# Performance work log

Measured on AMD Instinct MI355X. Metric: run time of the kernel, lower is better.

## Reference

```python
import jax, jax.numpy as jnp
import numpy as np

FEAT = 256
HID = FEAT // 2
N_KEYS = 2          # output_keys = ["energy_0", "energy_1"]
N_MOLS = 2000
ATOMS_PER_MOL = 100
N_ATOMS = N_MOLS * ATOMS_PER_MOL
LOG2 = 0.6931471805599453


def shifted_softplus(x):
    # NFF's shifted softplus: softplus(x) - log(2)
    return jax.nn.softplus(x) - LOG2


def setup_inputs() -> dict:
    key = jax.random.key(0)
    ks = jax.random.split(key, 6)
    s_i = jax.random.normal(ks[0], (N_ATOMS, FEAT), dtype=jnp.float32)
    xyz = jax.random.normal(ks[1], (N_ATOMS, 3), dtype=jnp.float32)
    num_atoms = jnp.full((N_MOLS,), ATOMS_PER_MOL, dtype=jnp.int64)
    # Per-key MLP params stacked over keys: Linear(F->H), act, Linear(H->1)
    W1 = jax.random.normal(ks[2], (N_KEYS, FEAT, HID), dtype=jnp.float32) / np.sqrt(FEAT)
    b1 = jnp.zeros((N_KEYS, HID), dtype=jnp.float32)
    W2 = jax.random.normal(ks[3], (N_KEYS, HID), dtype=jnp.float32) / np.sqrt(HID)
    b2 = jnp.zeros((N_KEYS,), dtype=jnp.float32)
    return {"s_i": s_i, "xyz": xyz, "num_atoms": num_atoms,
            "W1": W1, "b1": b1, "W2": W2, "b2": b2}


def reference(s_i, xyz, num_atoms, W1, b1, W2, b2):
    n_mols = num_atoms.shape[0]
    # segment id per atom, replacing the torch.split(...)+per-chunk sum loop
    seg = jnp.repeat(jnp.arange(n_mols), num_atoms,
                     total_repeat_length=s_i.shape[0])        # [N]
    # per-key MLP: [K,N,H] hidden, [K,N] scalar output per atom
    h = shifted_softplus(jnp.einsum('nf,kfh->knh', s_i, W1) + b1[:, None, :])
    val = jnp.einsum('knh,kh->kn', h, W2) + b2[:, None]       # [K, N]
    # fused segment-sum pooling -> per-molecule scalars
    pooled = jax.ops.segment_sum(val.T, seg, num_segments=n_mols)  # [M, K]
    return pooled.T                                            # [K, M]
```

## Files before the change

### kernel.cpp

```cpp
#include <hip/hip_runtime.h>

#define FEAT 256
#define HID 128
#define NKEYS 2

typedef __bf16 bf16x8 __attribute__((ext_vector_type(8)));
typedef float f32x16 __attribute__((ext_vector_type(16)));

union Frag {
    bf16x8 v;
    unsigned u[4];
    uint4 q;
};

__device__ __forceinline__ unsigned pack_bf16_2(float f0, float f1) {
    unsigned u0 = __float_as_uint(f0) + 0x8000u;
    unsigned u1 = __float_as_uint(f1) + 0x8000u;
    return __builtin_amdgcn_perm(u1, u0, 0x07060302u);
}

__device__ __forceinline__ float ssp(float x) {
    float sp = __logf(1.0f + __expf(x));
    sp = (x > 15.0f) ? x : sp;
    return sp - 0.69314718056f;
}

__device__ __forceinline__ int find_mol(const int* __restrict__ off, int n_mols, int g) {
    int lo = 0, hi = n_mols;
    while (hi - lo > 1) {
        int mid = (lo + hi) >> 1;
        if (off[mid] <= g) lo = mid; else hi = mid;
    }
    return lo;
}

__global__ void prep_kernel(const void* __restrict__ num_atoms_raw,
                            const float* __restrict__ W1,
                            int n_mols, int n_atoms,
                            int* __restrict__ off,
                            unsigned short* __restrict__ Bp,
                            float* __restrict__ out, int out_n) {
    if (blockIdx.x > 0) {
        int idx = (blockIdx.x - 1) * 256 + threadIdx.x;
        int c = idx >> 8;
        int k = idx & 255;
        int key = c >> 7, j = c & 127;
        float f = W1[(size_t)key * FEAT * HID + (size_t)k * HID + j];
        unsigned u = __float_as_uint(f);
        unsigned r = (u + 0x7FFFu + ((u >> 16) & 1u)) >> 16;
        Bp[(size_t)c * FEAT + k] = (unsigned short)r;
        return;
    }
    for (int i = threadIdx.x; i < out_n; i += 256) out[i] = 0.0f;

    __shared__ long long tsum[256];
    __shared__ int csum[257];
    __shared__ int mode_sh;
    int tid = threadIdx.x;
    const int* a32 = (const int*)num_atoms_raw;
    const long long* a64 = (const long long*)num_atoms_raw;
    int chunk = (n_mols + 255) >> 8;
    int lo = tid * chunk;
    if (lo > n_mols) lo = n_mols;
    int hi = lo + chunk;
    if (hi > n_mols) hi = n_mols;
    long long s = 0;
    for (int i = lo; i < hi; ++i) s += (long long)a32[i];
    tsum[tid] = s;
    __syncthreads();
    if (tid == 0) {
        long long t = 0;
        for (int i = 0; i < 256; ++i) t += tsum[i];
        mode_sh = (t == (long long)n_atoms) ? 0 : 1;
    }
    __syncthreads();
    int mode = mode_sh;
    if (mode) {
        s = 0;
        for (int i = lo; i < hi; ++i) s += a64[i];
        tsum[tid] = s;
    }
    csum[tid] = (int)tsum[tid];
    __syncthreads();
    if (tid == 0) {
        int run = 0;
        for (int i = 0; i < 256; ++i) { int v = csum[i]; csum[i] = run; run += v; }
    }
    __syncthreads();
    int run = csum[tid];
    for (int i = lo; i < hi; ++i) {
        off[i] = run;
        run += mode ? (int)a64[i] : a32[i];
    }
    if (hi >= n_mols) off[n_mols] = run;
}

__global__ __launch_bounds__(256, 2)
void gemm_fused(const float* __restrict__ A,
                const unsigned short* __restrict__ Bp,
                const float* __restrict__ b1,
                const float* __restrict__ W2,
                const float* __restrict__ b2,
                const int* __restrict__ off,
                float* __restrict__ out,
                int n_atoms, int n_mols) {
    __shared__ uint4 ldsA[4 * 64 * 8];
    __shared__ float part[4][64];
    __shared__ float molacc[NKEYS][4];

    const int tid  = threadIdx.x;
    const int lane = tid & 63;
    const int wn   = tid >> 6;
    const int l31  = lane & 31;
    const int half = lane >> 5;
    const int m0   = blockIdx.x * 64;

    const int srow = tid >> 2;
    const int sseg = tid & 3;
    int grow = m0 + srow;
    if (grow > n_atoms - 1) grow = n_atoms - 1;
    const float4* gsrc = (const float4*)(A + (size_t)grow * FEAT + sseg * 16);

    float4 fb[16];
    #pragma unroll
    for (int i = 0; i < 16; ++i)
        fb[i] = gsrc[(i >> 2) * 16 + (i & 3)];

    const int c0 = wn * 64 + l31;
    const unsigned short* bb0 = Bp + (size_t)c0 * FEAT + half * 8;
    const unsigned short* bb1 = Bp + (size_t)(c0 + 32) * FEAT + half * 8;
    Frag bf0[2][4], bf1[2][4];
    #pragma unroll
    for (int j = 0; j < 4; ++j) {
        bf0[0][j].q = *(const uint4*)(bb0 + j * 16);
        bf1[0][j].q = *(const uint4*)(bb1 + j * 16);
    }
    #pragma unroll
    for (int j = 0; j < 4; ++j) {
        bf0[1][j].q = *(const uint4*)(bb0 + 64 + j * 16);
        bf1[1][j].q = *(const uint4*)(bb1 + 64 + j * 16);
    }

    const int wb = srow * 8;
    const int rx = srow & 7;
    #pragma unroll
    for (int c = 0; c < 4; ++c) {
        float4 f0 = fb[c * 4 + 0], f1 = fb[c * 4 + 1];
        float4 f2 = fb[c * 4 + 2], f3 = fb[c * 4 + 3];
        uint4 p0, p1;
        p0.x = pack_bf16_2(f0.x, f0.y);
        p0.y = pack_bf16_2(f0.z, f0.w);
        p0.z = pack_bf16_2(f1.x, f1.y);
        p0.w = pack_bf16_2(f1.z, f1.w);
        p1.x = pack_bf16_2(f2.x, f2.y);
        p1.y = pack_bf16_2(f2.z, f2.w);
        p1.z = pack_bf16_2(f3.x, f3.y);
        p1.w = pack_bf16_2(f3.z, f3.w);
        ldsA[c * 512 + wb + ((sseg * 2)     ^ rx)] = p0;
        ldsA[c * 512 + wb + ((sseg * 2 + 1) ^ rx)] = p1;
    }
    __syncthreads();

    const int rb0 = l31 * 8;
    const int rb1 = (l31 + 32) * 8;
    const int rxor = l31 & 7;

    f32x16 acc00 = 0.0f, acc01 = 0.0f, acc10 = 0.0f, acc11 = 0.0f;

    #pragma unroll
    for (int c = 0; c < 4; ++c) {
        const int base = c * 512;
        const int slot = c & 1;
        #pragma unroll
        for (int j = 0; j < 4; ++j) {
            const int sw = (j * 2 + half) ^ rxor;
            Frag a0, a1;
            a0.q = ldsA[base + rb0 + sw];
            a1.q = ldsA[base + rb1 + sw];
            acc00 = __builtin_amdgcn_mfma_f32_32x32x16_bf16(a0.v, bf0[slot][j].v, acc00, 0, 0, 0);
            acc01 = __builtin_amdgcn_mfma_f32_32x32x16_bf16(a0.v, bf1[slot][j].v, acc01, 0, 0, 0);
            acc10 = __builtin_amdgcn_mfma_f32_32x32x16_bf16(a1.v, bf0[slot][j].v, acc10, 0, 0, 0);
            acc11 = __builtin_amdgcn_mfma_f32_32x32x16_bf16(a1.v, bf1[slot][j].v, acc11, 0, 0, 0);
        }
        if (c + 2 < 4) {
            const int kb = (c + 2) * 64;
            #pragma unroll
            for (int j = 0; j < 4; ++j) {
                bf0[slot][j].q = *(const uint4*)(bb0 + kb + j * 16);
                bf1[slot][j].q = *(const uint4*)(bb1 + kb + j * 16);
            }
        }
    }

    if (tid < NKEYS * 4) molacc[tid >> 2][tid & 3] = 0.0f;

    float b1c0 = b1[c0], b1c1 = b1[c0 + 32];
    float w2c0 = W2[c0], w2c1 = W2[c0 + 32];

    #pragma unroll
    for (int rt = 0; rt < 2; ++rt) {
        const f32x16& Ac0 = rt ? acc10 : acc00;
        const f32x16& Ac1 = rt ? acc11 : acc01;
        #pragma unroll
        for (int r = 0; r < 16; ++r) {
            float t = ssp(Ac0[r] + b1c0) * w2c0 + ssp(Ac1[r] + b1c1) * w2c1;
            t += __shfl_xor(t, 1);
            t += __shfl_xor(t, 2);
            t += __shfl_xor(t, 4);
            t += __shfl_xor(t, 8);
            t += __shfl_xor(t, 16);
            if (l31 == r) {
                int row = rt * 32 + (r & 3) + 8 * (r >> 2) + 4 * half;
                part[wn][row] = t;
            }
        }
    }
    __syncthreads();

    if (tid < NKEYS * 64) {
        int key = tid >> 6, r = tid & 63;
        int gm = m0 + r;
        if (gm < n_atoms) {
            float val = part[2 * key][r] + part[2 * key + 1][r] + b2[key];
            int mol  = find_mol(off, n_mols, gm);
            int mol0 = find_mol(off, n_mols, m0);
            int ml = mol - mol0;
            if (ml < 4) atomicAdd(&molacc[key][ml], val);
            else        atomicAdd(&out[(size_t)key * n_mols + mol], val);
        }
    }
    __syncthreads();

    if (tid < NKEYS * 4) {
        int key = tid >> 2, ml = tid & 3;
        int mol0 = find_mol(off, n_mols, m0);
        int mol = mol0 + ml;
        if (mol < n_mols) {
            float v = molacc[key][ml];
            if (v != 0.0f) atomicAdd(&out[(size_t)key * n_mols + mol], v);
        }
    }
}

extern "C" void kernel_launch(void* const* d_in, const int* in_sizes, int n_in,
                              void* d_out, int out_size, void* d_ws, size_t ws_size,
                              hipStream_t stream) {
    const float* s_i      = (const float*)d_in[0];
    const void*  num_atoms = d_in[2];
    const float* W1 = (const float*)d_in[3];
    const float* b1 = (const float*)d_in[4];
    const float* W2 = (const float*)d_in[5];
    const float* b2 = (const float*)d_in[6];
    int n_atoms = in_sizes[0] / FEAT;
    int n_mols  = in_sizes[2];
    float* out = (float*)d_out;

    int* off = (int*)d_ws;
    size_t off_bytes = (((size_t)(n_mols + 1) * 4) + 255) & ~(size_t)255;
    unsigned short* Bp = (unsigned short*)((char*)d_ws + off_bytes);

    int pack_blocks = (NKEYS * HID * FEAT) / 256;
    prep_kernel<<<1 + pack_blocks, 256, 0, stream>>>(num_atoms, W1, n_mols, n_atoms,
                                                     off, Bp, out, out_size);

    int gblocks = (n_atoms + 63) / 64;
    gemm_fused<<<gblocks, 256, 0, stream>>>(s_i, Bp, b1, W2, b2, off, out, n_atoms, n_mols);
}
```

Before: 350.6 us.

## Load fp32 activations straight to LDS with global_load_lds and convert to bf16 after

Replaces the register-staged A tile load (global to registers, bf16 pack, then LDS store) with direct global-to-LDS 16-byte loads of the fp32 rows. A rotated column layout avoids bank conflicts. The bf16 conversion moves into the MFMA loop, applied after each LDS read. This frees the registers that held the 16 float4 staging values and removes the separate pack/store phase. In exchange LDS use doubles to 64KB per block, which may reduce occupancy, and each LDS read in the inner loop is twice as wide.

```diff
diff --git a/kernel.cpp b/kernel.cpp
--- a/kernel.cpp
+++ b/kernel.cpp
@@ -13,9 +13,16 @@
     uint4 q;
 };
 
-__device__ __forceinline__ unsigned pack_bf16_2(float f0, float f1) {
-    unsigned u0 = __float_as_uint(f0) + 0x8000u;
-    unsigned u1 = __float_as_uint(f1) + 0x8000u;
+__device__ __forceinline__ void load_lds16(const float* g, void* l) {
+    __builtin_amdgcn_global_load_lds(
+        (const __attribute__((address_space(1))) unsigned int*)g,
+        (__attribute__((address_space(3))) unsigned int*)l,
+        16, 0, 0);
+}
+
+__device__ __forceinline__ unsigned pack_bf16_u2(unsigned u0, unsigned u1) {
+    u0 += 0x8000u;
+    u1 += 0x8000u;
     return __builtin_amdgcn_perm(u1, u0, 0x07060302u);
 }
 
@@ -104,7 +111,7 @@
                 const int* __restrict__ off,
                 float* __restrict__ out,
                 int n_atoms, int n_mols) {
-    __shared__ uint4 ldsA[4 * 64 * 8];
+    __shared__ uint4 ldsA[64 * 64];
     __shared__ float part[4][64];
     __shared__ float molacc[NKEYS][4];
 
@@ -115,68 +122,53 @@
     const int half = lane >> 5;
     const int m0   = blockIdx.x * 64;
 
-    const int srow = tid >> 2;
-    const int sseg = tid & 3;
-    int grow = m0 + srow;
-    if (grow > n_atoms - 1) grow = n_atoms - 1;
-    const float4* gsrc = (const float4*)(A + (size_t)grow * FEAT + sseg * 16);
-
-    float4 fb[16];
-    #pragma unroll
-    for (int i = 0; i < 16; ++i)
-        fb[i] = gsrc[(i >> 2) * 16 + (i & 3)];
+    #pragma unroll
+    for (int i = 0; i < 16; ++i) {
+        const int r = wn * 16 + i;
+        int grow = m0 + r;
+        if (grow > n_atoms - 1) grow = n_atoms - 1;
+        const float* gp = A + (size_t)grow * FEAT + (((lane - r) & 63) << 2);
+        load_lds16(gp, (void*)&ldsA[r * 64]);
+    }
 
     const int c0 = wn * 64 + l31;
     const unsigned short* bb0 = Bp + (size_t)c0 * FEAT + half * 8;
     const unsigned short* bb1 = Bp + (size_t)(c0 + 32) * FEAT + half * 8;
     Frag bf0[2][4], bf1[2][4];
     #pragma unroll
-    for (int j = 0; j < 4; ++j) {
-        bf0[0][j].q = *(const uint4*)(bb0 + j * 16);
-        bf1[0][j].q = *(const uint4*)(bb1 + j * 16);
-    }
-    #pragma unroll
-    for (int j = 0; j < 4; ++j) {
-        bf0[1][j].q = *(const uint4*)(bb0 + 64 + j * 16);
-        bf1[1][j].q = *(const uint4*)(bb1 + 64 + j * 16);
-    }
-
-    const int wb = srow * 8;
-    const int rx = srow & 7;
+    for (int s = 0; s < 2; ++s)
+        #pragma unroll
+        for (int j = 0; j < 4; ++j) {
+            bf0[s][j].q = *(const uint4*)(bb0 + s * 64 + j * 16);
+            bf1[s][j].q = *(const uint4*)(bb1 + s * 64 + j * 16);
+        }
+
+    __syncthreads();
+
+    const int rb0 = l31 * 64;
+    const int rb1 = (l31 + 32) * 64;
+
+    f32x16 acc00 = 0.0f, acc01 = 0.0f, acc10 = 0.0f, acc11 = 0.0f;
+
     #pragma unroll
     for (int c = 0; c < 4; ++c) {
-        float4 f0 = fb[c * 4 + 0], f1 = fb[c * 4 + 1];
-        float4 f2 = fb[c * 4 + 2], f3 = fb[c * 4 + 3];
-        uint4 p0, p1;
-        p0.x = pack_bf16_2(f0.x, f0.y);
-        p0.y = pack_bf16_2(f0.z, f0.w);
-        p0.z = pack_bf16_2(f1.x, f1.y);
-        p0.w = pack_bf16_2(f1.z, f1.w);
-        p1.x = pack_bf16_2(f2.x, f2.y);
-        p1.y = pack_bf16_2(f2.z, f2.w);
-        p1.z = pack_bf16_2(f3.x, f3.y);
-        p1.w = pack_bf16_2(f3.z, f3.w);
-        ldsA[c * 512 + wb + ((sseg * 2)     ^ rx)] = p0;
-        ldsA[c * 512 + wb + ((sseg * 2 + 1) ^ rx)] = p1;
-    }
-    __syncthreads();
-
-    const int rb0 = l31 * 8;
-    const int rb1 = (l31 + 32) * 8;
-    const int rxor = l31 & 7;
-
-    f32x16 acc00 = 0.0f, acc01 = 0.0f, acc10 = 0.0f, acc11 = 0.0f;
-
-    #pragma unroll
-    for (int c = 0; c < 4; ++c) {
-        const int base = c * 512;
         const int slot = c & 1;
         #pragma unroll
         for (int j = 0; j < 4; ++j) {
-            const int sw = (j * 2 + half) ^ rxor;
+            const int g0 = c * 16 + j * 4 + half * 2;
+            uint4 q0 = ldsA[rb0 + ((g0     + l31) & 63)];
+            uint4 q1 = ldsA[rb0 + ((g0 + 1 + l31) & 63)];
+            uint4 r0 = ldsA[rb1 + ((g0     + l31 + 32) & 63)];
+            uint4 r1 = ldsA[rb1 + ((g0 + 1 + l31 + 32) & 63)];
             Frag a0, a1;
-            a0.q = ldsA[base + rb0 + sw];
-            a1.q = ldsA[base + rb1 + sw];
+            a0.u[0] = pack_bf16_u2(q0.x, q0.y);
+            a0.u[1] = pack_bf16_u2(q0.z, q0.w);
+            a0.u[2] = pack_bf16_u2(q1.x, q1.y);
+            a0.u[3] = pack_bf16_u2(q1.z, q1.w);
+            a1.u[0] = pack_bf16_u2(r0.x, r0.y);
+            a1.u[1] = pack_bf16_u2(r0.z, r0.w);
+            a1.u[2] = pack_bf16_u2(r1.x, r1.y);
+            a1.u[3] = pack_bf16_u2(r1.z, r1.w);
             acc00 = __builtin_amdgcn_mfma_f32_32x32x16_bf16(a0.v, bf0[slot][j].v, acc00, 0, 0, 0);
             acc01 = __builtin_amdgcn_mfma_f32_32x32x16_bf16(a0.v, bf1[slot][j].v, acc01, 0, 0, 0);
             acc10 = __builtin_amdgcn_mfma_f32_32x32x16_bf16(a1.v, bf0[slot][j].v, acc10, 0, 0, 0);
```

Result: slower. 375.4 us (+7.1%).
